# Kernel tuning notes

Measured on AMD Instinct MI355X. Metric: run time of the kernel, lower is better.

Reference implementation:

```python
import jax, jax.numpy as jnp
import numpy as np

N = 131072   # total nodes
B = 256      # graphs
NPG = 512    # nodes per graph (N = B*NPG, nodes ordered by graph)
K = 7        # knn neighbors
H = 4        # heads


def setup_inputs() -> dict:
    key = jax.random.key(0)
    ks = jax.random.split(key, 16)
    s = 0.1
    pos = jax.random.normal(ks[0], (N, 3), jnp.float32)
    x = jax.random.normal(ks[1], (N, 10), jnp.float32)
    batch = jnp.repeat(jnp.arange(B, dtype=jnp.int32), NPG)
    # GATv2 layer 1: in=10, out=16, heads=4 -> H*C = 64
    Wl1 = jax.random.normal(ks[2], (10, 64), jnp.float32) * s
    bl1 = jnp.zeros((64,), jnp.float32)
    Wr1 = jax.random.normal(ks[3], (10, 64), jnp.float32) * s
    br1 = jnp.zeros((64,), jnp.float32)
    att1 = jax.random.normal(ks[4], (H, 16), jnp.float32) * s
    bias1 = jnp.zeros((64,), jnp.float32)
    # GATv2 layer 2: in=64, out=32, heads=4 -> H*C = 128
    Wl2 = jax.random.normal(ks[5], (64, 128), jnp.float32) * s
    bl2 = jnp.zeros((128,), jnp.float32)
    Wr2 = jax.random.normal(ks[6], (64, 128), jnp.float32) * s
    br2 = jnp.zeros((128,), jnp.float32)
    att2 = jax.random.normal(ks[7], (H, 32), jnp.float32) * s
    bias2 = jnp.zeros((128,), jnp.float32)
    return dict(pos=pos, x=x, batch=batch,
                Wl1=Wl1, bl1=bl1, Wr1=Wr1, br1=br1, att1=att1, bias1=bias1,
                Wl2=Wl2, bl2=bl2, Wr2=Wr2, br2=br2, att2=att2, bias2=bias2)


def knn_edges(pos):
    # equal-size graphs, nodes ordered by graph -> per-graph brute-force kNN
    p = pos.reshape(B, NPG, -1)                                  # [B,n,3]
    d2 = jnp.sum((p[:, :, None, :] - p[:, None, :, :]) ** 2, -1)  # [B,n,n]
    d2 = d2 + jnp.eye(NPG, dtype=d2.dtype) * 1e10                 # no self-loops
    _, idx = jax.lax.top_k(-d2, K)                                # [B,n,K]
    offs = (jnp.arange(B, dtype=idx.dtype) * NPG)[:, None, None]
    src = (idx + offs).reshape(-1)                                # neighbors -> sources
    dst = jnp.broadcast_to(jnp.arange(N)[:, None], (N, K)).reshape(-1)
    return src, dst


def gatv2(x, src, dst, Wl, bl, Wr, br, att, C):
    xl = (x @ Wl + bl).reshape(N, H, C)   # lin_l -> source features / messages
    xr = (x @ Wr + br).reshape(N, H, C)   # lin_r -> target features
    m = jax.nn.leaky_relu(xl[src] + xr[dst], 0.2)     # [E,H,C]
    alpha = jnp.einsum('ehc,hc->eh', m, att)          # [E,H]
    amax = jax.ops.segment_max(alpha, dst, num_segments=N)
    ea = jnp.exp(alpha - amax[dst])
    denom = jax.ops.segment_sum(ea, dst, num_segments=N)
    a = ea / denom[dst]                               # softmax per destination
    out = jax.ops.segment_sum(a[:, :, None] * xl[src], dst, num_segments=N)
    return out.reshape(N, H * C)


def reference(pos, x, batch, Wl1, bl1, Wr1, br1, att1, bias1,
              Wl2, bl2, Wr2, br2, att2, bias2):
    src, dst = knn_edges(pos)
    h = gatv2(x, src, dst, Wl1, bl1, Wr1, br1, att1, 16) + bias1   # [N,64]
    h = gatv2(h, src, dst, Wl2, bl2, Wr2, br2, att2, 32) + bias2   # [N,128]
    # global mean pool over batch ids
    sums = jax.ops.segment_sum(h, batch, num_segments=B)
    cnts = jax.ops.segment_sum(jnp.ones((N, 1), h.dtype), batch, num_segments=B)
    return sums / cnts                                              # [B,128]
```

## Files before the change

kernel.cpp:

```cpp
#include <hip/hip_runtime.h>
#include <hip/hip_bf16.h>

#define N_NODES 131072
#define B_GRAPHS 256
#define NPG 512
#define KNN 7
#define HEADS 4

using f4 = __attribute__((ext_vector_type(4))) float;
using short8 = __attribute__((ext_vector_type(8))) short;

__device__ __forceinline__ unsigned short f2bf(float f) {
    unsigned u = __builtin_bit_cast(unsigned, f);
    u += 0x7FFFu + ((u >> 16) & 1u);
    return (unsigned short)(u >> 16);
}

__device__ __forceinline__ void s8_to_f(const short8 v, f4* out) {
#pragma unroll
    for (int i = 0; i < 8; ++i) {
        const unsigned u = ((unsigned)(unsigned short)v[i]) << 16;
        out[i >> 2][i & 3] = __builtin_bit_cast(float, u);
    }
}

__global__ __launch_bounds__(256) void knn_kernel(const float* __restrict__ pos,
                                                  int* __restrict__ knn) {
    __shared__ f4 sp[NPG];
    const int tid = threadIdx.x;
    const int g = blockIdx.x >> 1;
    const int q = ((blockIdx.x & 1) << 8) | tid;

    const float* p = pos + (size_t)g * NPG * 3;
    for (int i = tid; i < NPG; i += 256) {
        f4 v; v[0] = p[i * 3 + 0]; v[1] = p[i * 3 + 1]; v[2] = p[i * 3 + 2]; v[3] = 0.f;
        sp[i] = v;
    }
    __syncthreads();

    const f4 qp = sp[q];
    unsigned b0 = ~0u, b1 = ~0u, b2 = ~0u, b3 = ~0u, b4 = ~0u, b5 = ~0u, b6 = ~0u;

#define CEU(a, b) { const unsigned _mn = min(a, b); b = max(a, b); a = _mn; }
#pragma unroll 4
    for (int j = 0; j < NPG; ++j) {
        const f4 c = sp[j];
        const float dx = qp[0] - c[0];
        const float dy = qp[1] - c[1];
        const float dz = qp[2] - c[2];
        const float d2 = dx * dx + dy * dy + dz * dz;
        unsigned key = (__builtin_bit_cast(unsigned, d2) & 0xFFFFFE00u) | (unsigned)j;
        key = (j == q) ? 0xFFFFFFFFu : key;
        b6 = min(b6, key);
        CEU(b5, b6) CEU(b4, b5) CEU(b3, b4) CEU(b2, b3) CEU(b1, b2) CEU(b0, b1)
    }
#undef CEU
    const int base = (g * NPG + q) * KNN;
    const int off = g * NPG;
    knn[base + 0] = off + (int)(b0 & 0x1FFu);
    knn[base + 1] = off + (int)(b1 & 0x1FFu);
    knn[base + 2] = off + (int)(b2 & 0x1FFu);
    knn[base + 3] = off + (int)(b3 & 0x1FFu);
    knn[base + 4] = off + (int)(b4 & 0x1FFu);
    knn[base + 5] = off + (int)(b5 & 0x1FFu);
    knn[base + 6] = off + (int)(b6 & 0x1FFu);
}

__global__ __launch_bounds__(256) void lin1_kernel(const float* __restrict__ x,
                                                   const float* __restrict__ Wl,
                                                   const float* __restrict__ bl,
                                                   const float* __restrict__ Wr,
                                                   const float* __restrict__ br,
                                                   float* __restrict__ xl1,
                                                   float* __restrict__ xr1) {
    const int idx = blockIdx.x * 256 + threadIdx.x;
    const int c4 = idx & 15;
    const size_t node = (size_t)(idx >> 4);
    const float* xrow = x + node * 10;
    f4 al = ((const f4*)bl)[c4];
    f4 ar = ((const f4*)br)[c4];
#pragma unroll
    for (int k = 0; k < 10; ++k) {
        const float xv = xrow[k];
        al += xv * ((const f4*)(Wl + k * 64))[c4];
        ar += xv * ((const f4*)(Wr + k * 64))[c4];
    }
    ((f4*)(xl1 + node * 64))[c4] = al;
    ((f4*)(xr1 + node * 64))[c4] = ar;
}

__global__ __launch_bounds__(256) void agg1_kernel(const float* __restrict__ xl,
                                                   const float* __restrict__ xr,
                                                   const int* __restrict__ knn,
                                                   const float* __restrict__ att,
                                                   const float* __restrict__ bias,
                                                   unsigned short* __restrict__ h1b) {
    const int x = blockIdx.x & 7;
    const int i = blockIdx.x >> 3;
    const int graph = x * 32 + (i >> 3);
    const int sub = i & 7;
    const int tid = threadIdx.x;
    const int h = tid & 3;
    const size_t node = (size_t)graph * NPG + sub * 64 + (tid >> 2);

    const int* nb = knn + node * KNN;
    int j[KNN];
#pragma unroll
    for (int k = 0; k < KNN; ++k) j[k] = nb[k];

    f4 xr4[4], at4[4];
    const f4* xrp = (const f4*)(xr + node * 64 + h * 16);
    const f4* atp = (const f4*)(att + h * 16);
#pragma unroll
    for (int i2 = 0; i2 < 4; ++i2) { xr4[i2] = xrp[i2]; at4[i2] = atp[i2]; }

    float alpha[KNN];
#pragma unroll
    for (int k = 0; k < KNN; ++k) {
        const f4* xlp = (const f4*)(xl + (size_t)j[k] * 64 + h * 16);
        float s = 0.f;
#pragma unroll
        for (int i2 = 0; i2 < 4; ++i2) {
            const f4 m = xlp[i2] + xr4[i2];
#pragma unroll
            for (int c = 0; c < 4; ++c) {
                float mm = m[c];
                mm = mm > 0.f ? mm : 0.2f * mm;
                s += mm * at4[i2][c];
            }
        }
        alpha[k] = s;
    }
    float amax = alpha[0];
#pragma unroll
    for (int k = 1; k < KNN; ++k) amax = fmaxf(amax, alpha[k]);
    float e[KNN];
    float denom = 0.f;
#pragma unroll
    for (int k = 0; k < KNN; ++k) { e[k] = expf(alpha[k] - amax); denom += e[k]; }
    const float rd = 1.f / denom;

    f4 o4[4];
#pragma unroll
    for (int i2 = 0; i2 < 4; ++i2) o4[i2] = 0.f;
#pragma unroll
    for (int k = 0; k < KNN; ++k) {
        const f4* xlp = (const f4*)(xl + (size_t)j[k] * 64 + h * 16);
#pragma unroll
        for (int i2 = 0; i2 < 4; ++i2) o4[i2] += e[k] * xlp[i2];
    }
    const f4* bp = (const f4*)(bias + h * 16);
    short8 r0, r1;
#pragma unroll
    for (int i2 = 0; i2 < 4; ++i2) {
        const f4 v = o4[i2] * rd + bp[i2];
#pragma unroll
        for (int c = 0; c < 4; ++c) {
            const unsigned short bv = f2bf(v[c]);
            const int e4 = i2 * 4 + c;
            if (e4 < 8) r0[e4] = (short)bv; else r1[e4 - 8] = (short)bv;
        }
    }
    short8* hp = (short8*)(h1b + node * 64 + h * 16);
    hp[0] = r0;
    hp[1] = r1;
}

__global__ __launch_bounds__(256) void wprep_kernel(const float* __restrict__ Wl,
                                                    const float* __restrict__ Wr,
                                                    unsigned short* __restrict__ wbf) {
    const int t = blockIdx.x * 256 + threadIdx.x;
    const int k = t >> 8;
    const int n = t & 255;
    const float v = (n < 128) ? Wl[k * 128 + n] : Wr[k * 128 + (n - 128)];
    wbf[((k >> 3) * 256 + n) * 8 + (k & 7)] = f2bf(v);
}

__global__ __launch_bounds__(256) void lin2_kernel(const unsigned short* __restrict__ h1b,
                                                   const unsigned short* __restrict__ wbf,
                                                   const float* __restrict__ bl,
                                                   const float* __restrict__ br,
                                                   unsigned short* __restrict__ xl2b,
                                                   unsigned short* __restrict__ xr2b) {
    const int tid = threadIdx.x;
    const int lane = tid & 63;
    const int w = tid >> 6;
    const size_t node0 = (size_t)blockIdx.x * 16;
    const int lm = lane & 15, lk = lane >> 4;

    const short8* hp = (const short8*)h1b;
    const short8 a0 = hp[(node0 + lm) * 8 + lk];
    const short8 a1 = hp[(node0 + lm) * 8 + lk + 4];

    const short8* wp = (const short8*)wbf;
#pragma unroll
    for (int t = 0; t < 4; ++t) {
        const int col = w * 64 + t * 16 + lm;
        const float bias = (col < 128) ? bl[col] : br[col - 128];
        f4 acc = {bias, bias, bias, bias};
        const short8 b0 = wp[lk * 256 + col];
        const short8 b1 = wp[(lk + 4) * 256 + col];
        acc = __builtin_amdgcn_mfma_f32_16x16x32_bf16(a0, b0, acc, 0, 0, 0);
        acc = __builtin_amdgcn_mfma_f32_16x16x32_bf16(a1, b1, acc, 0, 0, 0);
        unsigned short* dst = (col < 128) ? (xl2b + col) : (xr2b + (col - 128));
#pragma unroll
        for (int r = 0; r < 4; ++r)
            dst[(node0 + lk * 4 + r) * 128] = f2bf(acc[r]);
    }
}

__global__ __launch_bounds__(256) void agg2_pool_kernel(const unsigned short* __restrict__ xl2b,
                                                        const unsigned short* __restrict__ xr2b,
                                                        const int* __restrict__ knn,
                                                        const float* __restrict__ att,
                                                        float* __restrict__ partial) {
    const int x = blockIdx.x & 7;
    const int i = blockIdx.x >> 3;
    const int graph = x * 32 + (i >> 4);
    const int sub = i & 15;
    const int tid = threadIdx.x;
    const int lane = tid & 63;
    const int wv = tid >> 6;
    const int n8 = lane >> 3;
    const int h = (lane >> 1) & 3;
    const int half = lane & 1;
    const size_t node = (size_t)graph * NPG + sub * 32 + wv * 8 + n8;
    const int co = h * 32 + half * 16;

    const int* nb = knn + node * KNN;
    int j[KNN];
#pragma unroll
    for (int k = 0; k < KNN; ++k) j[k] = nb[k];

    f4 xr4[4], at4[4];
    {
        const short8* xrp = (const short8*)(xr2b + node * 128 + co);
        s8_to_f(xrp[0], &xr4[0]);
        s8_to_f(xrp[1], &xr4[2]);
        const f4* atp = (const f4*)(att + co);
#pragma unroll
        for (int i2 = 0; i2 < 4; ++i2) at4[i2] = atp[i2];
    }

    float alpha[KNN];
#pragma unroll
    for (int k = 0; k < KNN; ++k) {
        const short8* xlp = (const short8*)(xl2b + (size_t)j[k] * 128 + co);
        f4 xlv[4];
        s8_to_f(xlp[0], &xlv[0]);
        s8_to_f(xlp[1], &xlv[2]);
        float s = 0.f;
#pragma unroll
        for (int i2 = 0; i2 < 4; ++i2) {
            const f4 m = xlv[i2] + xr4[i2];
#pragma unroll
            for (int c = 0; c < 4; ++c) {
                float mm = m[c];
                mm = mm > 0.f ? mm : 0.2f * mm;
                s += mm * at4[i2][c];
            }
        }
        alpha[k] = s + __shfl_xor(s, 1);
    }
    float amax = alpha[0];
#pragma unroll
    for (int k = 1; k < KNN; ++k) amax = fmaxf(amax, alpha[k]);
    float e[KNN];
    float denom = 0.f;
#pragma unroll
    for (int k = 0; k < KNN; ++k) { e[k] = expf(alpha[k] - amax); denom += e[k]; }
    const float rd = 1.f / denom;

    f4 o4[4];
#pragma unroll
    for (int i2 = 0; i2 < 4; ++i2) o4[i2] = 0.f;
#pragma unroll
    for (int k = 0; k < KNN; ++k) {
        const short8* xlp = (const short8*)(xl2b + (size_t)j[k] * 128 + co);
        f4 xlv[4];
        s8_to_f(xlp[0], &xlv[0]);
        s8_to_f(xlp[1], &xlv[2]);
#pragma unroll
        for (int i2 = 0; i2 < 4; ++i2) o4[i2] += e[k] * xlv[i2];
    }
#pragma unroll
    for (int i2 = 0; i2 < 4; ++i2) o4[i2] *= rd;

#pragma unroll
    for (int m = 8; m <= 32; m <<= 1) {
#pragma unroll
        for (int i2 = 0; i2 < 4; ++i2) {
#pragma unroll
            for (int c = 0; c < 4; ++c) o4[i2][c] += __shfl_xor(o4[i2][c], m);
        }
    }
    if (n8 == 0) {
        f4* pp = (f4*)(partial + ((size_t)(graph * 16 + sub) * 4 + wv) * 128 + co);
#pragma unroll
        for (int i2 = 0; i2 < 4; ++i2) pp[i2] = o4[i2];
    }
}

__global__ __launch_bounds__(128) void pool2_kernel(const float* __restrict__ partial,
                                                    const float* __restrict__ bias,
                                                    float* __restrict__ out) {
    const int g = blockIdx.x;
    const int c = threadIdx.x;
    float s = 0.f;
#pragma unroll
    for (int b = 0; b < 64; ++b) s += partial[(size_t)(g * 64 + b) * 128 + c];
    out[g * 128 + c] = s * (1.f / 512.f) + bias[c];
}

extern "C" void kernel_launch(void* const* d_in, const int* in_sizes, int n_in,
                              void* d_out, int out_size, void* d_ws, size_t ws_size,
                              hipStream_t stream) {
    const float* pos   = (const float*)d_in[0];
    const float* x     = (const float*)d_in[1];
    const float* Wl1   = (const float*)d_in[3];
    const float* bl1   = (const float*)d_in[4];
    const float* Wr1   = (const float*)d_in[5];
    const float* br1   = (const float*)d_in[6];
    const float* att1  = (const float*)d_in[7];
    const float* bias1 = (const float*)d_in[8];
    const float* Wl2   = (const float*)d_in[9];
    const float* bl2   = (const float*)d_in[10];
    const float* Wr2   = (const float*)d_in[11];
    const float* br2   = (const float*)d_in[12];
    const float* att2  = (const float*)d_in[13];
    const float* bias2 = (const float*)d_in[14];
    float* out = (float*)d_out;

    char* ws = (char*)d_ws;
    int*            knn  = (int*)(ws + 0);
    float*          xl1  = (float*)(ws + 3670016);
    float*          xr1  = (float*)(ws + 37224448);
    unsigned short* h1b  = (unsigned short*)(ws + 70778880);
    unsigned short* wbf  = (unsigned short*)(ws + 87556096);
    unsigned short* xl2b = (unsigned short*)(ws + 88080384);
    unsigned short* xr2b = (unsigned short*)(ws + 121634816);
    float*          partial = (float*)(ws + 70778880);

    knn_kernel<<<N_NODES / 256, 256, 0, stream>>>(pos, knn);
    lin1_kernel<<<(N_NODES * 16) / 256, 256, 0, stream>>>(x, Wl1, bl1, Wr1, br1, xl1, xr1);
    wprep_kernel<<<64, 256, 0, stream>>>(Wl2, Wr2, wbf);
    agg1_kernel<<<(N_NODES * 4) / 256, 256, 0, stream>>>(xl1, xr1, knn, att1, bias1, h1b);
    lin2_kernel<<<N_NODES / 16, 256, 0, stream>>>(h1b, wbf, bl2, br2, xl2b, xr2b);
    agg2_pool_kernel<<<N_NODES / 32, 256, 0, stream>>>(xl2b, xr2b, knn, att2, partial);
    pool2_kernel<<<B_GRAPHS, 128, 0, stream>>>(partial, bias2, out);
}
```

Before: 179.8 us.

## Split kNN candidates across two thread halves and store layer-1 xl in bf16

```diff
diff --git a/kernel.cpp b/kernel.cpp
--- a/kernel.cpp
+++ b/kernel.cpp
@@ -24,54 +24,77 @@
     }
 }
 
-__global__ __launch_bounds__(256) void knn_kernel(const float* __restrict__ pos,
+#define INS7(B, KEY) { \
+    const unsigned _k = (KEY); \
+    const unsigned n0 = min(B[0], _k); \
+    const unsigned n1 = max(B[0], min(B[1], _k)); \
+    const unsigned n2 = max(B[1], min(B[2], _k)); \
+    const unsigned n3 = max(B[2], min(B[3], _k)); \
+    const unsigned n4 = max(B[3], min(B[4], _k)); \
+    const unsigned n5 = max(B[4], min(B[5], _k)); \
+    const unsigned n6 = max(B[5], min(B[6], _k)); \
+    B[0]=n0; B[1]=n1; B[2]=n2; B[3]=n3; B[4]=n4; B[5]=n5; B[6]=n6; }
+
+__global__ __launch_bounds__(512) void knn_kernel(const float* __restrict__ pos,
                                                   int* __restrict__ knn) {
     __shared__ f4 sp[NPG];
+    __shared__ unsigned mk[256 * 7];
     const int tid = threadIdx.x;
     const int g = blockIdx.x >> 1;
-    const int q = ((blockIdx.x & 1) << 8) | tid;
+    const int qh = blockIdx.x & 1;
+    const int ch = tid >> 8;
+    const int q = (qh << 8) | (tid & 255);
 
     const float* p = pos + (size_t)g * NPG * 3;
-    for (int i = tid; i < NPG; i += 256) {
-        f4 v; v[0] = p[i * 3 + 0]; v[1] = p[i * 3 + 1]; v[2] = p[i * 3 + 2]; v[3] = 0.f;
-        sp[i] = v;
+    {
+        f4 v; v[0] = p[tid * 3 + 0]; v[1] = p[tid * 3 + 1]; v[2] = p[tid * 3 + 2]; v[3] = 0.f;
+        sp[tid] = v;
     }
     __syncthreads();
 
     const f4 qp = sp[q];
-    unsigned b0 = ~0u, b1 = ~0u, b2 = ~0u, b3 = ~0u, b4 = ~0u, b5 = ~0u, b6 = ~0u;
-
-#define CEU(a, b) { const unsigned _mn = min(a, b); b = max(a, b); a = _mn; }
-#pragma unroll 4
-    for (int j = 0; j < NPG; ++j) {
-        const f4 c = sp[j];
+    unsigned b[7];
+#pragma unroll
+    for (int i = 0; i < 7; ++i) b[i] = 0xFFFFFFFFu;
+
+    const int j0 = ch << 8;
+#pragma unroll 8
+    for (int j = 0; j < 256; ++j) {
+        const int jj = j0 + j;
+        const f4 c = sp[jj];
         const float dx = qp[0] - c[0];
         const float dy = qp[1] - c[1];
         const float dz = qp[2] - c[2];
         const float d2 = dx * dx + dy * dy + dz * dz;
-        unsigned key = (__builtin_bit_cast(unsigned, d2) & 0xFFFFFE00u) | (unsigned)j;
-        key = (j == q) ? 0xFFFFFFFFu : key;
-        b6 = min(b6, key);
-        CEU(b5, b6) CEU(b4, b5) CEU(b3, b4) CEU(b2, b3) CEU(b1, b2) CEU(b0, b1)
-    }
-#undef CEU
-    const int base = (g * NPG + q) * KNN;
-    const int off = g * NPG;
-    knn[base + 0] = off + (int)(b0 & 0x1FFu);
-    knn[base + 1] = off + (int)(b1 & 0x1FFu);
-    knn[base + 2] = off + (int)(b2 & 0x1FFu);
-    knn[base + 3] = off + (int)(b3 & 0x1FFu);
-    knn[base + 4] = off + (int)(b4 & 0x1FFu);
-    knn[base + 5] = off + (int)(b5 & 0x1FFu);
-    knn[base + 6] = off + (int)(b6 & 0x1FFu);
-}
+        unsigned key = (__builtin_bit_cast(unsigned, d2) & 0xFFFFFE00u) | (unsigned)jj;
+        key = (jj == q) ? 0xFFFFFFFFu : key;
+        INS7(b, key)
+    }
+
+    if (ch == 1) {
+        unsigned* m = &mk[(tid & 255) * 7];
+#pragma unroll
+        for (int i = 0; i < 7; ++i) m[i] = b[i];
+    }
+    __syncthreads();
+    if (ch == 0) {
+        const unsigned* m = &mk[tid * 7];
+#pragma unroll
+        for (int i = 0; i < 7; ++i) INS7(b, m[i])
+        const int base = (g * NPG + q) * KNN;
+        const int off = g * NPG;
+#pragma unroll
+        for (int i = 0; i < 7; ++i) knn[base + i] = off + (int)(b[i] & 0x1FFu);
+    }
+}
+#undef INS7
 
 __global__ __launch_bounds__(256) void lin1_kernel(const float* __restrict__ x,
                                                    const float* __restrict__ Wl,
                                                    const float* __restrict__ bl,
                                                    const float* __restrict__ Wr,
                                                    const float* __restrict__ br,
-                                                   float* __restrict__ xl1,
+                                                   unsigned short* __restrict__ xl1b,
                                                    float* __restrict__ xr1) {
     const int idx = blockIdx.x * 256 + threadIdx.x;
     const int c4 = idx & 15;
@@ -85,11 +108,14 @@
         al += xv * ((const f4*)(Wl + k * 64))[c4];
         ar += xv * ((const f4*)(Wr + k * 64))[c4];
     }
-    ((f4*)(xl1 + node * 64))[c4] = al;
+    uint2 pk;
+    pk.x = (unsigned)f2bf(al[0]) | ((unsigned)f2bf(al[1]) << 16);
+    pk.y = (unsigned)f2bf(al[2]) | ((unsigned)f2bf(al[3]) << 16);
+    ((uint2*)xl1b)[node * 16 + c4] = pk;
     ((f4*)(xr1 + node * 64))[c4] = ar;
 }
 
-__global__ __launch_bounds__(256) void agg1_kernel(const float* __restrict__ xl,
+__global__ __launch_bounds__(256) void agg1_kernel(const unsigned short* __restrict__ xl1b,
                                                    const float* __restrict__ xr,
                                                    const int* __restrict__ knn,
                                                    const float* __restrict__ att,
@@ -117,11 +143,14 @@
     float alpha[KNN];
 #pragma unroll
     for (int k = 0; k < KNN; ++k) {
-        const f4* xlp = (const f4*)(xl + (size_t)j[k] * 64 + h * 16);
+        const short8* xlp = (const short8*)(xl1b + (size_t)j[k] * 64 + h * 16);
+        f4 xlv[4];
+        s8_to_f(xlp[0], &xlv[0]);
+        s8_to_f(xlp[1], &xlv[2]);
         float s = 0.f;
 #pragma unroll
         for (int i2 = 0; i2 < 4; ++i2) {
-            const f4 m = xlp[i2] + xr4[i2];
+            const f4 m = xlv[i2] + xr4[i2];
 #pragma unroll
             for (int c = 0; c < 4; ++c) {
                 float mm = m[c];
@@ -145,9 +174,12 @@
     for (int i2 = 0; i2 < 4; ++i2) o4[i2] = 0.f;
 #pragma unroll
     for (int k = 0; k < KNN; ++k) {
-        const f4* xlp = (const f4*)(xl + (size_t)j[k] * 64 + h * 16);
-#pragma unroll
-        for (int i2 = 0; i2 < 4; ++i2) o4[i2] += e[k] * xlp[i2];
+        const short8* xlp = (const short8*)(xl1b + (size_t)j[k] * 64 + h * 16);
+        f4 xlv[4];
+        s8_to_f(xlp[0], &xlv[0]);
+        s8_to_f(xlp[1], &xlv[2]);
+#pragma unroll
+        for (int i2 = 0; i2 < 4; ++i2) o4[i2] += e[k] * xlv[i2];
     }
     const f4* bp = (const f4*)(bias + h * 16);
     short8 r0, r1;
@@ -333,18 +365,18 @@
 
     char* ws = (char*)d_ws;
     int*            knn  = (int*)(ws + 0);
-    float*          xl1  = (float*)(ws + 3670016);
-    float*          xr1  = (float*)(ws + 37224448);
-    unsigned short* h1b  = (unsigned short*)(ws + 70778880);
-    unsigned short* wbf  = (unsigned short*)(ws + 87556096);
+    unsigned short* xl1b = (unsigned short*)(ws + 3670016);
+    float*          xr1  = (float*)(ws + 20447232);
+    unsigned short* h1b  = (unsigned short*)(ws + 54001664);
+    unsigned short* wbf  = (unsigned short*)(ws + 70778880);
     unsigned short* xl2b = (unsigned short*)(ws + 88080384);
     unsigned short* xr2b = (unsigned short*)(ws + 121634816);
-    float*          partial = (float*)(ws + 70778880);
-
-    knn_kernel<<<N_NODES / 256, 256, 0, stream>>>(pos, knn);
-    lin1_kernel<<<(N_NODES * 16) / 256, 256, 0, stream>>>(x, Wl1, bl1, Wr1, br1, xl1, xr1);
+    float*          partial = (float*)(ws + 54001664);
+
+    knn_kernel<<<B_GRAPHS * 2, 512, 0, stream>>>(pos, knn);
+    lin1_kernel<<<(N_NODES * 16) / 256, 256, 0, stream>>>(x, Wl1, bl1, Wr1, br1, xl1b, xr1);
     wprep_kernel<<<64, 256, 0, stream>>>(Wl2, Wr2, wbf);
-    agg1_kernel<<<(N_NODES * 4) / 256, 256, 0, stream>>>(xl1, xr1, knn, att1, bias1, h1b);
+    agg1_kernel<<<(N_NODES * 4) / 256, 256, 0, stream>>>(xl1b, xr1, knn, att1, bias1, h1b);
     lin2_kernel<<<N_NODES / 16, 256, 0, stream>>>(h1b, wbf, bl2, br2, xl2b, xr2b);
     agg2_pool_kernel<<<N_NODES / 32, 256, 0, stream>>>(xl2b, xr2b, knn, att2, partial);
     pool2_kernel<<<B_GRAPHS, 128, 0, stream>>>(partial, bias2, out);
```

Measured after the change: 167.5 us. 6.9% less time.
